# Kernel tuning notes

Measured on AMD Instinct MI355X. Metric: run time of the kernel, lower is better.

Reference implementation:

```python
import jax, jax.numpy as jnp
import numpy as np

K_DIM = 1024
HEADS = 16


def setup_inputs() -> dict:
    key = jax.random.key(0)
    ks = jax.random.split(key, 8)
    b, t, tc, k = 2, 2048, 2048, K_DIM
    scale = 1.0 / np.sqrt(k)
    x = jax.random.normal(ks[0], (b, t, k), dtype=jnp.float32)
    context = jax.random.normal(ks[1], (b, tc, k), dtype=jnp.float32)
    Wq = jax.random.normal(ks[2], (k, k), dtype=jnp.float32) * scale
    Wk = jax.random.normal(ks[3], (k, k), dtype=jnp.float32) * scale
    Wv = jax.random.normal(ks[4], (k, k), dtype=jnp.float32) * scale
    Wo = jax.random.normal(ks[5], (k, k), dtype=jnp.float32) * scale
    bo = jax.random.normal(ks[6], (k,), dtype=jnp.float32) * 0.01
    return {"x": x, "context": context, "Wq": Wq, "Wk": Wk, "Wv": Wv, "Wo": Wo, "bo": bo}


def reference(x, context, Wq, Wk, Wv, Wo, bo):
    b, t, e = x.shape
    tc = context.shape[1]
    h = HEADS
    s = e // h
    # Linear(k,k,bias=False): y = x @ W.T
    q = (x @ Wq.T).reshape(b, t, h, s)
    k_ = (context @ Wk.T).reshape(b, tc, h, s)
    v = (context @ Wv.T).reshape(b, tc, h, s)
    # scale q and k each by e**-0.25 (net 1/sqrt(e), note: full embed dim, not head dim)
    inv4 = e ** (-0.25)
    q = q * inv4
    k_ = k_ * inv4
    # scores: [b, h, t, tc]
    dot = jnp.einsum('bthd,bchd->bhtc', q, k_)
    attn = jax.nn.softmax(dot, axis=-1)
    out = jnp.einsum('bhtc,bchd->bthd', attn, v).reshape(b, t, e)
    return out @ Wo.T + bo
```

## Files before the change

### kernel.cpp

```cpp
#include <hip/hip_runtime.h>
#include <stdint.h>

typedef unsigned short u16;
typedef unsigned int u32;
typedef __attribute__((ext_vector_type(4))) float f32x4;
typedef __attribute__((ext_vector_type(16))) float f32x16;
typedef __attribute__((ext_vector_type(8))) __bf16 bf16x8;
typedef __attribute__((ext_vector_type(8))) u16 u16x8;

constexpr int NB = 2, NT = 2048, NTC = 2048, NE = 1024, NH = 16, ND = 64;
constexpr int MTOK = NB * NT;
constexpr int KDIM = NE;
constexpr float QK_SCALE = (float)(0.17677669529663687 * 1.2011224087864498);
constexpr float FIXED_M = 24.0f;

__device__ __forceinline__ u16 f2bf(float f) {
  union { float f; uint32_t u; } v; v.f = f;
  uint32_t r = v.u + 0x7FFFu + ((v.u >> 16) & 1u);
  return (u16)(r >> 16);
}

__device__ __forceinline__ float fexp2(float x) {
#if __has_builtin(__builtin_amdgcn_exp2f)
  return __builtin_amdgcn_exp2f(x);
#else
  return exp2f(x);
#endif
}

__device__ __forceinline__ u32 cvtpk(float lo, float hi) {
  u32 r;
  asm("v_cvt_pk_bf16_f32 %0, %1, %2" : "=v"(r) : "v"(lo), "v"(hi));
  return r;
}

__device__ __forceinline__ void plswap(u32& a, u32& b) {
  asm("v_permlane32_swap_b32 %0, %1" : "+v"(a), "+v"(b));
}

__device__ __forceinline__ void gload16(const void* g, void* lds) {
  __builtin_amdgcn_global_load_lds(
      (const __attribute__((address_space(1))) unsigned int*)g,
      (__attribute__((address_space(3))) unsigned int*)lds, 16, 0, 0);
}

__device__ __forceinline__ f32x4 mfma16x16(bf16x8 a, bf16x8 b, f32x4 c) {
  return __builtin_amdgcn_mfma_f32_16x16x32_bf16(a, b, c, 0, 0, 0);
}
__device__ __forceinline__ f32x16 mfma32x32(bf16x8 a, bf16x8 b, f32x16 c) {
  return __builtin_amdgcn_mfma_f32_32x32x16_bf16(a, b, c, 0, 0, 0);
}

__device__ __forceinline__ int swz(int row, int part) {
  return row * 128 + ((part ^ (row & 7)) << 4);
}

__device__ __forceinline__ u16x8 cast8(const float4* p, float scale) {
  float4 a = p[0], b = p[1];
  u16x8 r;
  r[0] = f2bf(a.x * scale); r[1] = f2bf(a.y * scale);
  r[2] = f2bf(a.z * scale); r[3] = f2bf(a.w * scale);
  r[4] = f2bf(b.x * scale); r[5] = f2bf(b.y * scale);
  r[6] = f2bf(b.z * scale); r[7] = f2bf(b.w * scale);
  return r;
}

__global__ void cast_xc(const float* __restrict__ a, const float* __restrict__ bp,
                        u16* __restrict__ oa, u16* __restrict__ ob, int n8each) {
  int i = blockIdx.x * blockDim.x + threadIdx.x;
  const float* src = (i < n8each) ? a : bp;
  u16* dst = (i < n8each) ? oa : ob;
  int j = (i < n8each) ? i : i - n8each;
  *((u16x8*)dst + j) = cast8((const float4*)src + (size_t)j * 2, 1.0f);
}

__global__ void cast_w(const float* __restrict__ w0, const float* __restrict__ w1,
                       const float* __restrict__ w2, const float* __restrict__ w3,
                       u16* __restrict__ out) {
  int i = blockIdx.x * blockDim.x + threadIdx.x;
  int which = i >> 17, j = i & 131071;
  const float* src = (which == 0) ? w0 : (which == 1) ? w1 : (which == 2) ? w2 : w3;
  float scale = (which < 2) ? QK_SCALE : 1.0f;
  u16* dst = out + (size_t)which * (NE * KDIM);
  *((u16x8*)dst + j) = cast8((const float4*)src + (size_t)j * 2, scale);
}

template <int MODE>
__global__ __launch_bounds__(256)
void gemm_bt(const u16* __restrict__ A, const u16* __restrict__ Bm,
             void* __restrict__ Cout, const float* __restrict__ bias) {
  __shared__ __align__(16) u16 Al[64 * 64];
  __shared__ __align__(16) u16 Bl[128 * 64];
  const int tid = threadIdx.x, w = tid >> 6, l = tid & 63;
  const int l15 = l & 15, l4 = l >> 4;
  const int wm = w >> 1, wn = w & 1;
  const int mbase = blockIdx.y * 64, nbase = blockIdx.x * 128;

  f32x4 acc[2][4] = {};

  const char* Ab = (const char*)(A + (size_t)mbase * KDIM);
  const char* Bb = (const char*)(Bm + (size_t)nbase * KDIM);

  for (int k0 = 0; k0 < KDIM; k0 += 64) {
#pragma unroll
    for (int s = 0; s < 2; ++s) {
      int i = (w * 2 + s) * 64 + l;
      int row = i >> 3, part = i & 7;
      int gofs = row * (KDIM * 2) + k0 * 2 + ((part ^ (row & 7)) << 4);
      gload16(Ab + gofs, (char*)Al + (w * 2 + s) * 1024);
    }
#pragma unroll
    for (int s = 0; s < 4; ++s) {
      int i = (w * 4 + s) * 64 + l;
      int row = i >> 3, part = i & 7;
      int gofs = row * (KDIM * 2) + k0 * 2 + ((part ^ (row & 7)) << 4);
      gload16(Bb + gofs, (char*)Bl + (w * 4 + s) * 1024);
    }
    __syncthreads();
#pragma unroll
    for (int kc = 0; kc < 2; ++kc) {
      bf16x8 af[2], bfr[4];
#pragma unroll
      for (int mt = 0; mt < 2; ++mt) {
        int r = wm * 32 + mt * 16 + l15;
        af[mt] = *(const bf16x8*)((const char*)Al + swz(r, kc * 4 + l4));
      }
#pragma unroll
      for (int nt = 0; nt < 4; ++nt) {
        int r = wn * 64 + nt * 16 + l15;
        bfr[nt] = *(const bf16x8*)((const char*)Bl + swz(r, kc * 4 + l4));
      }
#pragma unroll
      for (int mt = 0; mt < 2; ++mt)
#pragma unroll
        for (int nt = 0; nt < 4; ++nt)
          acc[mt][nt] = mfma16x16(af[mt], bfr[nt], acc[mt][nt]);
    }
    __syncthreads();
  }

#pragma unroll
  for (int mt = 0; mt < 2; ++mt) {
#pragma unroll
    for (int nt = 0; nt < 4; ++nt) {
      int col = nbase + wn * 64 + nt * 16 + l15;
      int mrow0 = mbase + wm * 32 + mt * 16 + l4 * 4;
#pragma unroll
      for (int r = 0; r < 4; ++r) {
        int m = mrow0 + r;
        float v = acc[mt][nt][r];
        if (MODE == 0) {
          int b = m >> 11, t = m & (NT - 1), h = col >> 6, d = col & (ND - 1);
          ((u16*)Cout)[((size_t)(b * NH + h) * NT + t) * ND + d] = f2bf(v);
        } else if (MODE == 3) {
          int b = m >> 11, tc = m & (NTC - 1), h = col >> 6, d = col & (ND - 1);
          size_t idx = ((size_t)((b * NH + h) * 32 + (tc >> 6))) * 4096
                     + (size_t)(d >> 3) * 512 + (size_t)(tc & 63) * 8 + (d & 7);
          ((u16*)Cout)[idx] = f2bf(v);
        } else if (MODE == 1) {
          int h = m >> 6, d = m & (ND - 1), b = col >> 11, tc = col & (NTC - 1);
          size_t idx = ((size_t)((b * NH + h) * 32 + (tc >> 6))) * 4096
                     + (size_t)((tc & 63) >> 3) * 512 + (size_t)d * 8 + (tc & 7);
          ((u16*)Cout)[idx] = f2bf(v);
        } else {
          ((float*)Cout)[(size_t)m * NE + col] = v + bias[col];
        }
      }
    }
  }
}

__global__ __launch_bounds__(128, 3)
void attn_fwd(const u16* __restrict__ Q, const u16* __restrict__ K,
              const u16* __restrict__ Vt, u16* __restrict__ O) {
  __shared__ float Ol[32 * 64];
  __shared__ float Ll[32];
  const int tid = threadIdx.x, wid = tid >> 6, l = tid & 63;
  const int l31 = l & 31, hi = l >> 5;

  int n = blockIdx.x;
  int work = (n & 7) * 256 + (n >> 3);
  const int bh = work >> 6, qx = work & 63;
  const int b = bh >> 4, h = bh & 15;
  const int qbase = qx * 32;

  const char* Kb = (const char*)(K + (size_t)bh * 32 * 4096);
  const char* Vb = (const char*)(Vt + (size_t)bh * 32 * 4096);
  const u16* Qb = Q + (size_t)bh * NT * ND;

  auto kaddr = [&](int t32, int kc) {
    return Kb + (size_t)(t32 >> 1) * 8192 + (size_t)(kc * 2 + hi) * 1024
              + (size_t)((t32 & 1) * 32 + l31) * 16;
  };
  auto vaddr = [&](int t32, int j) {
    return Vb + (size_t)(t32 >> 1) * 8192
              + (size_t)((t32 & 1) * 4 + (j >> 1) * 2 + hi) * 1024
              + (size_t)((j & 1) * 32 + l31) * 16;
  };

  bf16x8 qf[4];
#pragma unroll
  for (int kc = 0; kc < 4; ++kc)
    qf[kc] = *(const bf16x8*)(Qb + (size_t)(qbase + l31) * ND + kc * 16 + hi * 8);

  f32x16 oacc0 = {}, oacc1 = {}, lacc = {};
  f32x16 minit;
#pragma unroll
  for (int r = 0; r < 16; ++r) minit[r] = -FIXED_M;

  const int tbase = wid * 32;

  bf16x8 kfA[4], kfB[4], vf[4];
#pragma unroll
  for (int kc = 0; kc < 4; ++kc) kfA[kc] = *(const bf16x8*)kaddr(tbase, kc);

  for (int it2 = 0; it2 < 16; ++it2) {
    const int tA = tbase + it2 * 2, tB = tA + 1;

#pragma unroll
    for (int j = 0; j < 4; ++j) vf[j] = *(const bf16x8*)vaddr(tA, j);
#pragma unroll
    for (int kc = 0; kc < 4; ++kc) kfB[kc] = *(const bf16x8*)kaddr(tB, kc);
    {
      f32x16 sv = minit;
#pragma unroll
      for (int kc = 0; kc < 4; ++kc) sv = mfma32x32(kfA[kc], qf[kc], sv);
#pragma unroll
      for (int r = 0; r < 16; ++r) { sv[r] = fexp2(sv[r]); lacc[r] += sv[r]; }
      bf16x8 pa0, pa1;
      {
        u32 a1 = cvtpk(sv[0], sv[1]), b1 = cvtpk(sv[4], sv[5]);
        u32 a2 = cvtpk(sv[2], sv[3]), b2 = cvtpk(sv[6], sv[7]);
        plswap(a1, b1); plswap(a2, b2);
        u32 a3 = cvtpk(sv[8], sv[9]), b3 = cvtpk(sv[12], sv[13]);
        u32 a4 = cvtpk(sv[10], sv[11]), b4 = cvtpk(sv[14], sv[15]);
        plswap(a3, b3); plswap(a4, b4);
        union { u32 u[4]; bf16x8 v; } ua, ub;
        ua.u[0] = a1; ua.u[1] = a2; ua.u[2] = b1; ua.u[3] = b2;
        ub.u[0] = a3; ub.u[1] = a4; ub.u[2] = b3; ub.u[3] = b4;
        pa0 = ua.v; pa1 = ub.v;
      }
      oacc0 = mfma32x32(pa0, vf[0], oacc0);
      oacc1 = mfma32x32(pa0, vf[1], oacc1);
      oacc0 = mfma32x32(pa1, vf[2], oacc0);
      oacc1 = mfma32x32(pa1, vf[3], oacc1);
    }

#pragma unroll
    for (int j = 0; j < 4; ++j) vf[j] = *(const bf16x8*)vaddr(tB, j);
#pragma unroll
    for (int kc = 0; kc < 4; ++kc) kfA[kc] = *(const bf16x8*)kaddr(tB + 1, kc);
    {
      f32x16 sv = minit;
#pragma unroll
      for (int kc = 0; kc < 4; ++kc) sv = mfma32x32(kfB[kc], qf[kc], sv);
#pragma unroll
      for (int r = 0; r < 16; ++r) { sv[r] = fexp2(sv[r]); lacc[r] += sv[r]; }
      bf16x8 pa0, pa1;
      {
        u32 a1 = cvtpk(sv[0], sv[1]), b1 = cvtpk(sv[4], sv[5]);
        u32 a2 = cvtpk(sv[2], sv[3]), b2 = cvtpk(sv[6], sv[7]);
        plswap(a1, b1); plswap(a2, b2);
        u32 a3 = cvtpk(sv[8], sv[9]), b3 = cvtpk(sv[12], sv[13]);
        u32 a4 = cvtpk(sv[10], sv[11]), b4 = cvtpk(sv[14], sv[15]);
        plswap(a3, b3); plswap(a4, b4);
        union { u32 u[4]; bf16x8 v; } ua, ub;
        ua.u[0] = a1; ua.u[1] = a2; ua.u[2] = b1; ua.u[3] = b2;
        ub.u[0] = a3; ub.u[1] = a4; ub.u[2] = b3; ub.u[3] = b4;
        pa0 = ua.v; pa1 = ub.v;
      }
      oacc0 = mfma32x32(pa0, vf[0], oacc0);
      oacc1 = mfma32x32(pa0, vf[1], oacc1);
      oacc0 = mfma32x32(pa1, vf[2], oacc0);
      oacc1 = mfma32x32(pa1, vf[3], oacc1);
    }
  }

  float lsum;
  {
    f32x16 t = lacc;
#pragma unroll
    for (int s = 8; s >= 1; s >>= 1)
#pragma unroll
      for (int r = 0; r < s; ++r) t[r] += t[r + s];
    lsum = t[0] + __shfl_xor(t[0], 32);
  }

  if (wid == 1) {
#pragma unroll
    for (int r = 0; r < 16; ++r) {
      int crow = (r & 3) + 8 * (r >> 2) + 4 * hi;
      Ol[crow * 64 + l31] = oacc0[r];
      Ol[crow * 64 + 32 + l31] = oacc1[r];
    }
    if (!hi) Ll[l31] = lsum;
  }
  __syncthreads();
  if (wid == 0) {
    float inv = 1.0f / (lsum + Ll[l31]);
#pragma unroll
    for (int r = 0; r < 16; ++r) {
      int crow = (r & 3) + 8 * (r >> 2) + 4 * hi;
      float ir = __shfl(inv, crow);
      int t = qbase + crow;
      size_t rowo = (size_t)(b * NT + t) * NE + h * 64 + l31;
      O[rowo] = f2bf((oacc0[r] + Ol[crow * 64 + l31]) * ir);
      O[rowo + 32] = f2bf((oacc1[r] + Ol[crow * 64 + 32 + l31]) * ir);
    }
  }
}

extern "C" void kernel_launch(void* const* d_in, const int* in_sizes, int n_in,
                              void* d_out, int out_size, void* d_ws, size_t ws_size,
                              hipStream_t stream) {
  const float* x   = (const float*)d_in[0];
  const float* ctx = (const float*)d_in[1];
  const float* Wq  = (const float*)d_in[2];
  const float* Wk  = (const float*)d_in[3];
  const float* Wv  = (const float*)d_in[4];
  const float* Wo  = (const float*)d_in[5];
  const float* bo  = (const float*)d_in[6];
  float* out = (float*)d_out;
  char* ws = (char*)d_ws;

  u16* xb  = (u16*)(ws);
  u16* cb  = (u16*)(ws + (8u  << 20));
  u16* wqb = (u16*)(ws + (16u << 20));
  u16* wvb = (u16*)(ws + (20u << 20));
  u16* wob = (u16*)(ws + (22u << 20));
  u16* Qb  = (u16*)(ws + (24u << 20));
  u16* Kb  = (u16*)(ws + (32u << 20));
  u16* Vtb = (u16*)(ws + (40u << 20));
  u16* Ob  = (u16*)(ws + (48u << 20));
  u16* wkb = (u16*)(ws + (18u << 20));

  cast_xc<<<4096, 256, 0, stream>>>(x, ctx, xb, cb, MTOK * KDIM / 8);
  cast_w<<<2048, 256, 0, stream>>>(Wq, Wk, Wv, Wo, wqb);

  gemm_bt<0><<<dim3(8, 64), 256, 0, stream>>>(xb, wqb, Qb, nullptr);
  gemm_bt<3><<<dim3(8, 64), 256, 0, stream>>>(cb, wkb, Kb, nullptr);
  gemm_bt<1><<<dim3(32, 16), 256, 0, stream>>>(wvb, cb, Vtb, nullptr);

  attn_fwd<<<2048, 128, 0, stream>>>(Qb, Kb, Vtb, Ob);

  gemm_bt<2><<<dim3(8, 64), 256, 0, stream>>>(Ob, wob, out, bo);
}
```

Measured before the change: 134.1 us.

## Fuse K/V projections into one GEMM and double attention query tile per block

The separate K and V projection GEMMs become one GEMM over the concatenated Wk/Wv weights, with a mode that writes K in its tiled layout and V transposed into the adjacent buffer. This saves a launch and a second pass over the context activations. The attention kernel now processes 64 query rows per block (two 32-row tiles), so each loaded K/V fragment is reused twice and half as many blocks are launched. In exchange, register pressure roughly doubles for accumulators and Q fragments, and the occupancy hint drops from 3 to 2 blocks per CU.

```diff
diff --git a/kernel.cpp b/kernel.cpp
--- a/kernel.cpp
+++ b/kernel.cpp
@@ -152,16 +152,17 @@
         if (MODE == 0) {
           int b = m >> 11, t = m & (NT - 1), h = col >> 6, d = col & (ND - 1);
           ((u16*)Cout)[((size_t)(b * NH + h) * NT + t) * ND + d] = f2bf(v);
-        } else if (MODE == 3) {
-          int b = m >> 11, tc = m & (NTC - 1), h = col >> 6, d = col & (ND - 1);
-          size_t idx = ((size_t)((b * NH + h) * 32 + (tc >> 6))) * 4096
-                     + (size_t)(d >> 3) * 512 + (size_t)(tc & 63) * 8 + (d & 7);
-          ((u16*)Cout)[idx] = f2bf(v);
-        } else if (MODE == 1) {
-          int h = m >> 6, d = m & (ND - 1), b = col >> 11, tc = col & (NTC - 1);
-          size_t idx = ((size_t)((b * NH + h) * 32 + (tc >> 6))) * 4096
-                     + (size_t)((tc & 63) >> 3) * 512 + (size_t)d * 8 + (tc & 7);
-          ((u16*)Cout)[idx] = f2bf(v);
+        } else if (MODE == 4) {
+          int b = m >> 11, tc = m & (NTC - 1);
+          int h = (col >> 6) & 15, d = col & (ND - 1);
+          size_t base = ((size_t)((b * NH + h) * 32 + (tc >> 6))) * 4096;
+          if (col < 1024) {
+            size_t idx = base + (size_t)(d >> 3) * 512 + (size_t)(tc & 63) * 8 + (d & 7);
+            ((u16*)Cout)[idx] = f2bf(v);
+          } else {
+            size_t idx = base + (size_t)((tc & 63) >> 3) * 512 + (size_t)d * 8 + (tc & 7);
+            ((u16*)Cout)[4194304 + idx] = f2bf(v);
+          }
         } else {
           ((float*)Cout)[(size_t)m * NE + col] = v + bias[col];
         }
@@ -170,19 +171,19 @@
   }
 }
 
-__global__ __launch_bounds__(128, 3)
+__global__ __launch_bounds__(128, 2)
 void attn_fwd(const u16* __restrict__ Q, const u16* __restrict__ K,
               const u16* __restrict__ Vt, u16* __restrict__ O) {
-  __shared__ float Ol[32 * 64];
-  __shared__ float Ll[32];
+  __shared__ float Ol[64 * 64];
+  __shared__ float Ll[64];
   const int tid = threadIdx.x, wid = tid >> 6, l = tid & 63;
   const int l31 = l & 31, hi = l >> 5;
 
   int n = blockIdx.x;
-  int work = (n & 7) * 256 + (n >> 3);
-  const int bh = work >> 6, qx = work & 63;
+  int work = (n & 7) * 128 + (n >> 3);
+  const int bh = work >> 5, qx = work & 31;
   const int b = bh >> 4, h = bh & 15;
-  const int qbase = qx * 32;
+  const int qbase = qx * 64;
 
   const char* Kb = (const char*)(K + (size_t)bh * 32 * 4096);
   const char* Vb = (const char*)(Vt + (size_t)bh * 32 * 4096);
@@ -198,12 +199,15 @@
               + (size_t)((j & 1) * 32 + l31) * 16;
   };
 
-  bf16x8 qf[4];
-#pragma unroll
-  for (int kc = 0; kc < 4; ++kc)
-    qf[kc] = *(const bf16x8*)(Qb + (size_t)(qbase + l31) * ND + kc * 16 + hi * 8);
-
-  f32x16 oacc0 = {}, oacc1 = {}, lacc = {};
+  bf16x8 qf[2][4];
+#pragma unroll
+  for (int qt = 0; qt < 2; ++qt)
+#pragma unroll
+    for (int kc = 0; kc < 4; ++kc)
+      qf[qt][kc] = *(const bf16x8*)(Qb + (size_t)(qbase + qt * 32 + l31) * ND + kc * 16 + hi * 8);
+
+  f32x16 oacc[2][2] = {};
+  f32x16 lacc[2] = {};
   f32x16 minit;
 #pragma unroll
   for (int r = 0; r < 16; ++r) minit[r] = -FIXED_M;
@@ -221,12 +225,13 @@
     for (int j = 0; j < 4; ++j) vf[j] = *(const bf16x8*)vaddr(tA, j);
 #pragma unroll
     for (int kc = 0; kc < 4; ++kc) kfB[kc] = *(const bf16x8*)kaddr(tB, kc);
-    {
+#pragma unroll
+    for (int qt = 0; qt < 2; ++qt) {
       f32x16 sv = minit;
 #pragma unroll
-      for (int kc = 0; kc < 4; ++kc) sv = mfma32x32(kfA[kc], qf[kc], sv);
-#pragma unroll
-      for (int r = 0; r < 16; ++r) { sv[r] = fexp2(sv[r]); lacc[r] += sv[r]; }
+      for (int kc = 0; kc < 4; ++kc) sv = mfma32x32(kfA[kc], qf[qt][kc], sv);
+#pragma unroll
+      for (int r = 0; r < 16; ++r) { sv[r] = fexp2(sv[r]); lacc[qt][r] += sv[r]; }
       bf16x8 pa0, pa1;
       {
         u32 a1 = cvtpk(sv[0], sv[1]), b1 = cvtpk(sv[4], sv[5]);
@@ -240,22 +245,23 @@
         ub.u[0] = a3; ub.u[1] = a4; ub.u[2] = b3; ub.u[3] = b4;
         pa0 = ua.v; pa1 = ub.v;
       }
-      oacc0 = mfma32x32(pa0, vf[0], oacc0);
-      oacc1 = mfma32x32(pa0, vf[1], oacc1);
-      oacc0 = mfma32x32(pa1, vf[2], oacc0);
-      oacc1 = mfma32x32(pa1, vf[3], oacc1);
+      oacc[qt][0] = mfma32x32(pa0, vf[0], oacc[qt][0]);
+      oacc[qt][1] = mfma32x32(pa0, vf[1], oacc[qt][1]);
+      oacc[qt][0] = mfma32x32(pa1, vf[2], oacc[qt][0]);
+      oacc[qt][1] = mfma32x32(pa1, vf[3], oacc[qt][1]);
     }
 
 #pragma unroll
     for (int j = 0; j < 4; ++j) vf[j] = *(const bf16x8*)vaddr(tB, j);
 #pragma unroll
     for (int kc = 0; kc < 4; ++kc) kfA[kc] = *(const bf16x8*)kaddr(tB + 1, kc);
-    {
+#pragma unroll
+    for (int qt = 0; qt < 2; ++qt) {
       f32x16 sv = minit;
 #pragma unroll
-      for (int kc = 0; kc < 4; ++kc) sv = mfma32x32(kfB[kc], qf[kc], sv);
-#pragma unroll
-      for (int r = 0; r < 16; ++r) { sv[r] = fexp2(sv[r]); lacc[r] += sv[r]; }
+      for (int kc = 0; kc < 4; ++kc) sv = mfma32x32(kfB[kc], qf[qt][kc], sv);
+#pragma unroll
+      for (int r = 0; r < 16; ++r) { sv[r] = fexp2(sv[r]); lacc[qt][r] += sv[r]; }
       bf16x8 pa0, pa1;
       {
         u32 a1 = cvtpk(sv[0], sv[1]), b1 = cvtpk(sv[4], sv[5]);
@@ -269,43 +275,50 @@
         ub.u[0] = a3; ub.u[1] = a4; ub.u[2] = b3; ub.u[3] = b4;
         pa0 = ua.v; pa1 = ub.v;
       }
-      oacc0 = mfma32x32(pa0, vf[0], oacc0);
-      oacc1 = mfma32x32(pa0, vf[1], oacc1);
-      oacc0 = mfma32x32(pa1, vf[2], oacc0);
-      oacc1 = mfma32x32(pa1, vf[3], oacc1);
-    }
-  }
-
-  float lsum;
-  {
-    f32x16 t = lacc;
+      oacc[qt][0] = mfma32x32(pa0, vf[0], oacc[qt][0]);
+      oacc[qt][1] = mfma32x32(pa0, vf[1], oacc[qt][1]);
+      oacc[qt][0] = mfma32x32(pa1, vf[2], oacc[qt][0]);
+      oacc[qt][1] = mfma32x32(pa1, vf[3], oacc[qt][1]);
+    }
+  }
+
+  float lsum[2];
+#pragma unroll
+  for (int qt = 0; qt < 2; ++qt) {
+    f32x16 t = lacc[qt];
 #pragma unroll
     for (int s = 8; s >= 1; s >>= 1)
 #pragma unroll
       for (int r = 0; r < s; ++r) t[r] += t[r + s];
-    lsum = t[0] + __shfl_xor(t[0], 32);
+    lsum[qt] = t[0] + __shfl_xor(t[0], 32);
   }
 
   if (wid == 1) {
 #pragma unroll
-    for (int r = 0; r < 16; ++r) {
-      int crow = (r & 3) + 8 * (r >> 2) + 4 * hi;
-      Ol[crow * 64 + l31] = oacc0[r];
-      Ol[crow * 64 + 32 + l31] = oacc1[r];
-    }
-    if (!hi) Ll[l31] = lsum;
+    for (int qt = 0; qt < 2; ++qt) {
+#pragma unroll
+      for (int r = 0; r < 16; ++r) {
+        int crow = (r & 3) + 8 * (r >> 2) + 4 * hi;
+        Ol[(qt * 32 + crow) * 64 + l31] = oacc[qt][0][r];
+        Ol[(qt * 32 + crow) * 64 + 32 + l31] = oacc[qt][1][r];
+      }
+      if (!hi) Ll[qt * 32 + l31] = lsum[qt];
+    }
   }
   __syncthreads();
   if (wid == 0) {
-    float inv = 1.0f / (lsum + Ll[l31]);
-#pragma unroll
-    for (int r = 0; r < 16; ++r) {
-      int crow = (r & 3) + 8 * (r >> 2) + 4 * hi;
-      float ir = __shfl(inv, crow);
-      int t = qbase + crow;
-      size_t rowo = (size_t)(b * NT + t) * NE + h * 64 + l31;
-      O[rowo] = f2bf((oacc0[r] + Ol[crow * 64 + l31]) * ir);
-      O[rowo + 32] = f2bf((oacc1[r] + Ol[crow * 64 + 32 + l31]) * ir);
+#pragma unroll
+    for (int qt = 0; qt < 2; ++qt) {
+      float inv = 1.0f / (lsum[qt] + Ll[qt * 32 + l31]);
+#pragma unroll
+      for (int r = 0; r < 16; ++r) {
+        int crow = (r & 3) + 8 * (r >> 2) + 4 * hi;
+        float ir = __shfl(inv, crow);
+        int t = qbase + qt * 32 + crow;
+        size_t rowo = (size_t)(b * NT + t) * NE + h * 64 + l31;
+        O[rowo] = f2bf((oacc[qt][0][r] + Ol[(qt * 32 + crow) * 64 + l31]) * ir);
+        O[rowo + 32] = f2bf((oacc[qt][1][r] + Ol[(qt * 32 + crow) * 64 + 32 + l31]) * ir);
+      }
     }
   }
 }
@@ -326,22 +339,20 @@
   u16* xb  = (u16*)(ws);
   u16* cb  = (u16*)(ws + (8u  << 20));
   u16* wqb = (u16*)(ws + (16u << 20));
-  u16* wvb = (u16*)(ws + (20u << 20));
+  u16* wkb = (u16*)(ws + (18u << 20));
   u16* wob = (u16*)(ws + (22u << 20));
   u16* Qb  = (u16*)(ws + (24u << 20));
   u16* Kb  = (u16*)(ws + (32u << 20));
   u16* Vtb = (u16*)(ws + (40u << 20));
   u16* Ob  = (u16*)(ws + (48u << 20));
-  u16* wkb = (u16*)(ws + (18u << 20));
 
   cast_xc<<<4096, 256, 0, stream>>>(x, ctx, xb, cb, MTOK * KDIM / 8);
   cast_w<<<2048, 256, 0, stream>>>(Wq, Wk, Wv, Wo, wqb);
 
   gemm_bt<0><<<dim3(8, 64), 256, 0, stream>>>(xb, wqb, Qb, nullptr);
-  gemm_bt<3><<<dim3(8, 64), 256, 0, stream>>>(cb, wkb, Kb, nullptr);
-  gemm_bt<1><<<dim3(32, 16), 256, 0, stream>>>(wvb, cb, Vtb, nullptr);
-
-  attn_fwd<<<2048, 128, 0, stream>>>(Qb, Kb, Vtb, Ob);
+  gemm_bt<4><<<dim3(16, 64), 256, 0, stream>>>(cb, wkb, Kb, nullptr);
+
+  attn_fwd<<<1024, 128, 0, stream>>>(Qb, Kb, Vtb, Ob);
 
   gemm_bt<2><<<dim3(8, 64), 256, 0, stream>>>(Ob, wob, out, bo);
 }
```

New measurement: 122.3 us. 1.1x faster.
